# Optimization experiments

Hardware: AMD Instinct MI355X
Metric: run time of the kernel (lower is better)

## Reference

```python
import jax, jax.numpy as jnp
import numpy as np
import math

NUM_CLASSES = 100000
EMBED = 384
BATCH = 512
S = 64.0
M = 0.5
COS_M = math.cos(M)
SIN_M = math.sin(M)
TH = math.cos(math.pi - M)
MM = math.sin(math.pi - M) * M
EPS = 1e-07


def setup_inputs() -> dict:
    key = jax.random.key(0)
    k1, k2, k3 = jax.random.split(key, 3)
    embeddings = jax.random.normal(k1, (BATCH, EMBED), dtype=jnp.float32)
    labels = jax.random.randint(k2, (BATCH,), 0, NUM_CLASSES, dtype=jnp.int64)
    # xavier_uniform-like init for weight [num_classes, embedding_size]
    limit = math.sqrt(6.0 / (NUM_CLASSES + EMBED))
    weight = jax.random.uniform(k3, (NUM_CLASSES, EMBED), dtype=jnp.float32,
                                minval=-limit, maxval=limit)
    return {"embeddings": embeddings, "labels": labels, "weight": weight}


def reference(embeddings, labels, weight):
    # normalize class weights (note: embeddings are NOT normalized, per source)
    W = weight / jnp.linalg.norm(weight, axis=1, keepdims=True)  # [C, E]
    cos_theta = jnp.clip(embeddings @ W.T, -1.0 + EPS, 1.0 - EPS)  # [B, C]
    sin_theta = jnp.sqrt(1.0 - cos_theta ** 2)
    cos_theta_m = cos_theta * COS_M - sin_theta * SIN_M
    cos_theta_m = jnp.where(cos_theta > TH, cos_theta_m, cos_theta - MM)
    one_hot = jax.nn.one_hot(labels, cos_theta.shape[1], dtype=cos_theta.dtype)
    logits = S * (one_hot * cos_theta_m + (1.0 - one_hot) * cos_theta)
    # mean cross-entropy
    logp = jax.nn.log_softmax(logits, axis=-1)  # [B, C]
    nll = -jnp.take_along_axis(logp, labels[:, None], axis=1)[:, 0]
    return jnp.mean(nll)
```

## Files before the change

kernel.cpp:

```cpp
#include <hip/hip_runtime.h>
#include <hip/hip_bf16.h>
#include <math.h>

#define C_CLASSES 100000
#define EMBED     384
#define BATCH     512
#define S_SCALE   64.0f
#define COS_M_    0.8775825618903728f
#define SIN_M_    0.479425538604203f
#define TH_       (-0.8775825618903728f)
#define MM_       0.2397127693021015f
#define EPS_      1e-7f
#define LOG2E_    1.4426950408889634f
#define LN2_      0.6931471805599453f
#define BIGZ_     92.33261191693459f
#define SK1_      92.33248f

#define CT    32
#define NCHK  3125
#define NBLK  (NCHK * 2)

typedef __attribute__((ext_vector_type(8))) short bf16x8;
typedef __attribute__((ext_vector_type(4))) float f32x4;

__device__ inline ushort f2bf(float f) {
    unsigned u = __float_as_uint(f);
    unsigned r = (u + 0x7fffu + ((u >> 16) & 1u)) >> 16;
    return (ushort)r;
}

__global__ __launch_bounds__(256)
void cvt_pack_e(const float* __restrict__ emb, ushort* __restrict__ eP)
{
    int t = blockIdx.x * 256 + threadIdx.x;
    int lane = t & 63;
    int grp  = t >> 6;
    int tile = grp / 12, ks = grp % 12;
    int lr = lane & 15, lg = lane >> 4;
    int row = tile * 16 + lr;
    int col = ks * 32 + lg * 8;
    const float4* src = (const float4*)(emb + (size_t)row * EMBED + col);
    float4 v0 = src[0], v1 = src[1];
    ushort4 o0, o1;
    o0.x = f2bf(v0.x); o0.y = f2bf(v0.y); o0.z = f2bf(v0.z); o0.w = f2bf(v0.w);
    o1.x = f2bf(v1.x); o1.y = f2bf(v1.y); o1.z = f2bf(v1.z); o1.w = f2bf(v1.w);
    ((ushort4*)eP)[t * 2]     = o0;
    ((ushort4*)eP)[t * 2 + 1] = o1;
}

__global__ __launch_bounds__(256, 5)
void arc_fused32(const ushort* __restrict__ eP, const int* __restrict__ labels,
                 const float* __restrict__ weight,
                 float* __restrict__ psum, float* __restrict__ zlabel)
{
    __shared__ ushort Bl[(CT / 16) * 12 * 512];
    __shared__ int    labL[256];

    const int tid = threadIdx.x;

    const int orig = blockIdx.x;
    const int xcd  = orig & 7;
    const int qq   = NBLK >> 3, rr = NBLK & 7;
    const int bid  = (xcd < rr ? xcd * (qq + 1)
                               : rr * (qq + 1) + (xcd - rr) * qq) + (orig >> 3);
    const int ck   = bid >> 1;
    const int mh   = bid & 1;
    const int c0   = ck * CT;

    labL[tid] = labels[mh * 256 + tid];

    {
        const int p = tid & 15;
        #pragma unroll
        for (int h = 0; h < 2; ++h) {
            const int c = h * 16 + (tid >> 4);
            const float4* src =
                (const float4*)(weight + (size_t)(c0 + c) * EMBED) + p;

            float4 wv[6];
            float ss = 0.f;
            #pragma unroll
            for (int i = 0; i < 6; ++i) {
                wv[i] = src[16 * i];
                ss += wv[i].x * wv[i].x + wv[i].y * wv[i].y
                    + wv[i].z * wv[i].z + wv[i].w * wv[i].w;
            }
            ss += __shfl_xor(ss, 1, 64);
            ss += __shfl_xor(ss, 2, 64);
            ss += __shfl_xor(ss, 4, 64);
            ss += __shfl_xor(ss, 8, 64);
            const float inv = (ss > 0.f) ? rsqrtf(ss) : 0.f;

            const int t2 = c >> 4, cl = c & 15;
            #pragma unroll
            for (int i = 0; i < 6; ++i) {
                int q   = p + 16 * i;
                int ks  = q >> 3;
                int lgp = (q >> 1) & 3;
                int jo  = (q & 1) * 4;
                ushort4 o;
                o.x = f2bf(wv[i].x * inv); o.y = f2bf(wv[i].y * inv);
                o.z = f2bf(wv[i].z * inv); o.w = f2bf(wv[i].w * inv);
                int ei = (((t2 * 12 + ks) * 64) + cl + 16 * lgp) * 8 + jo;
                ei ^= (lgp & 3) << 4;
                *(ushort4*)&Bl[ei] = o;
            }
            __builtin_amdgcn_sched_barrier(0);
        }
    }
    __syncthreads();

    const int wid = tid >> 6, l = tid & 63;
    const int lr  = l & 15,  lg = l >> 4;
    const int bxo = (lg & 3) << 4;

    const ushort* abase = eP + ((size_t)((mh * 16 + wid * 4) * 12) * 64 + l) * 8;

    f32x4 acc[4][2];
    #pragma unroll
    for (int mt = 0; mt < 4; ++mt) {
        acc[mt][0] = (f32x4){0.f, 0.f, 0.f, 0.f};
        acc[mt][1] = (f32x4){0.f, 0.f, 0.f, 0.f};
    }

    #pragma unroll
    for (int ks = 0; ks < 12; ++ks) {
        bf16x8 a[4], b[2];
        #pragma unroll
        for (int mt = 0; mt < 4; ++mt)
            a[mt] = *(const bf16x8*)(abase + (mt * 12 + ks) * 512);
        #pragma unroll
        for (int nt = 0; nt < 2; ++nt) {
            int ei = ((nt * 12 + ks) * 64 + l) * 8;
            b[nt] = *(const bf16x8*)&Bl[ei ^ bxo];
        }
        #pragma unroll
        for (int mt = 0; mt < 4; ++mt) {
            acc[mt][0] = __builtin_amdgcn_mfma_f32_16x16x32_bf16(
                a[mt], b[0], acc[mt][0], 0, 0, 0);
            acc[mt][1] = __builtin_amdgcn_mfma_f32_16x16x32_bf16(
                a[mt], b[1], acc[mt][1], 0, 0, 0);
        }
    }

    #pragma unroll
    for (int mt = 0; mt < 4; ++mt) {
        #pragma unroll
        for (int rg = 0; rg < 4; ++rg) {
            const int rl  = wid * 64 + mt * 16 + lg * 4 + rg;
            const int r   = mh * 256 + rl;
            const int lab = labL[rl];
            float acc4 = 0.f;
            #pragma unroll
            for (int nt = 0; nt < 2; ++nt) {
                float cv = acc[mt][nt][rg];
                cv = fminf(fmaxf(cv, -1.f + EPS_), 1.f - EPS_);
                acc4 += exp2f(fmaf(cv, SK1_, -BIGZ_));
            }
            int off = lab - c0;
            if (((unsigned)off < 32u) && ((off & 15) == lr)) {
                float cv = (off >> 4) ? acc[mt][1][rg] : acc[mt][0][rg];
                cv = fminf(fmaxf(cv, -1.f + EPS_), 1.f - EPS_);
                float plain = exp2f(fmaf(cv, SK1_, -BIGZ_));
                float zm;
                if (cv > TH_) {
                    float sv = sqrtf(fmaxf(1.f - cv * cv, 0.f));
                    zm = S_SCALE * (cv * COS_M_ - sv * SIN_M_);
                } else {
                    zm = S_SCALE * (cv - MM_);
                }
                acc4 += exp2f(fmaf(zm, LOG2E_, -BIGZ_)) - plain;
                zlabel[r] = zm;
            }
            acc4 += __shfl_xor(acc4, 1, 64);
            acc4 += __shfl_xor(acc4, 2, 64);
            acc4 += __shfl_xor(acc4, 4, 64);
            acc4 += __shfl_xor(acc4, 8, 64);
            if (lr == 0) psum[(size_t)ck * BATCH + r] = acc4;
        }
    }
}

__global__ __launch_bounds__(256)
void arc_reduce(const float* __restrict__ psum, const float* __restrict__ zlabel,
                float* __restrict__ rowloss)
{
    const int r = blockIdx.x;
    const int tid = threadIdx.x;
    float s = 0.f;
    for (int k = tid; k < NCHK; k += 256)
        s += psum[(size_t)k * BATCH + r];
    #pragma unroll
    for (int d = 1; d < 64; d <<= 1) s += __shfl_xor(s, d, 64);
    __shared__ float ssh[4];
    if ((tid & 63) == 0) ssh[tid >> 6] = s;
    __syncthreads();
    if (tid == 0) {
        float t = ssh[0] + ssh[1] + ssh[2] + ssh[3];
        rowloss[r] = LN2_ * (BIGZ_ + log2f(t)) - zlabel[r];
    }
}

__global__ __launch_bounds__(512)
void arc_mean(const float* __restrict__ rowloss, float* __restrict__ out)
{
    const int tid = threadIdx.x;
    float v = rowloss[tid];
    #pragma unroll
    for (int d = 1; d < 64; d <<= 1) v += __shfl_xor(v, d, 64);
    __shared__ float sv[8];
    if ((tid & 63) == 0) sv[tid >> 6] = v;
    __syncthreads();
    if (tid == 0) {
        float t = 0.f;
        #pragma unroll
        for (int w = 0; w < 8; ++w) t += sv[w];
        out[0] = t / (float)BATCH;
    }
}

extern "C" void kernel_launch(void* const* d_in, const int* in_sizes, int n_in,
                              void* d_out, int out_size, void* d_ws, size_t ws_size,
                              hipStream_t stream)
{
    (void)in_sizes; (void)n_in; (void)out_size; (void)ws_size;
    const float* emb    = (const float*)d_in[0];
    const int*   labels = (const int*)d_in[1];
    const float* weight = (const float*)d_in[2];
    float* out = (float*)d_out;

    float*  psum    = (float*)d_ws;
    float*  zlabel  = psum + (size_t)NCHK * BATCH;
    float*  rowloss = zlabel + BATCH;
    ushort* eP      = (ushort*)(rowloss + BATCH);

    cvt_pack_e<<<(BATCH * EMBED / 8) / 256, 256, 0, stream>>>(emb, eP);
    arc_fused32<<<NBLK, 256, 0, stream>>>(eP, labels, weight, psum, zlabel);
    arc_reduce<<<BATCH, 256, 0, stream>>>(psum, zlabel, rowloss);
    arc_mean<<<1, 512, 0, stream>>>(rowloss, out);
}
```

Before: 102.6 us.

## Make weight GEMM kernel persistent with double-buffered global-to-LDS prefetch

Replaces the 6250-block one-shot kernel with 256 persistent blocks of 512 threads. Each block loops over class chunks and covers all 512 batch rows per chunk. Weight chunks are streamed straight into LDS with global_load_lds into two buffers, so the next chunk loads while the current one is normalised and multiplied. This is meant to hide global memory latency and cut launch and redundant weight-normalisation overhead. In exchange it uses about 124KB of LDS per block, which leaves one block per CU and relies on hand-placed waitcnt and barrier ordering. It also swaps the manual bf16 rounding for the library conversion.

```diff
diff --git a/kernel.cpp b/kernel.cpp
--- a/kernel.cpp
+++ b/kernel.cpp
@@ -18,15 +18,23 @@
 
 #define CT    32
 #define NCHK  3125
-#define NBLK  (NCHK * 2)
+#define NB    256
 
 typedef __attribute__((ext_vector_type(8))) short bf16x8;
 typedef __attribute__((ext_vector_type(4))) float f32x4;
+
+#define AS1 __attribute__((address_space(1)))
+#define AS3 __attribute__((address_space(3)))
 
 __device__ inline ushort f2bf(float f) {
     unsigned u = __float_as_uint(f);
     unsigned r = (u + 0x7fffu + ((u >> 16) & 1u)) >> 16;
     return (ushort)r;
+}
+
+__device__ inline ushort cvt_bf(float f) {
+    __hip_bfloat16 h = __float2bfloat16(f);
+    return *(ushort*)&h;
 }
 
 __global__ __launch_bounds__(256)
@@ -48,40 +56,60 @@
     ((ushort4*)eP)[t * 2 + 1] = o1;
 }
 
-__global__ __launch_bounds__(256, 5)
-void arc_fused32(const ushort* __restrict__ eP, const int* __restrict__ labels,
-                 const float* __restrict__ weight,
-                 float* __restrict__ psum, float* __restrict__ zlabel)
-{
+__global__ __launch_bounds__(512, 4)
+void arc_pipe32(const ushort* __restrict__ eP, const int* __restrict__ labels,
+                const float* __restrict__ weight,
+                float* __restrict__ psum, float* __restrict__ zlabel)
+{
+    __shared__ float  Raw[2][CT * EMBED];
     __shared__ ushort Bl[(CT / 16) * 12 * 512];
-    __shared__ int    labL[256];
+    __shared__ int    labL[BATCH];
 
     const int tid = threadIdx.x;
-
-    const int orig = blockIdx.x;
-    const int xcd  = orig & 7;
-    const int qq   = NBLK >> 3, rr = NBLK & 7;
-    const int bid  = (xcd < rr ? xcd * (qq + 1)
-                               : rr * (qq + 1) + (xcd - rr) * qq) + (orig >> 3);
-    const int ck   = bid >> 1;
-    const int mh   = bid & 1;
-    const int c0   = ck * CT;
-
-    labL[tid] = labels[mh * 256 + tid];
-
-    {
-        const int p = tid & 15;
-        #pragma unroll
-        for (int h = 0; h < 2; ++h) {
-            const int c = h * 16 + (tid >> 4);
-            const float4* src =
-                (const float4*)(weight + (size_t)(c0 + c) * EMBED) + p;
-
+    const int blk = blockIdx.x;
+    const int nch = 12 + ((blk < (NCHK - 12 * NB)) ? 1 : 0);
+
+    labL[tid] = labels[tid];
+
+    const int c  = tid >> 4, p = tid & 15;
+    const int t2 = c >> 4,  cl = c & 15;
+    const int wid = tid >> 6, l = tid & 63;
+    const int lr  = l & 15,  lg = l >> 4;
+    const int bxo = (lg & 3) << 4;
+    const ushort* abase = eP + ((size_t)(wid * 4) * 12 * 64 + l) * 8;
+
+#define DMA(CH, BUF) do {                                                     \
+        const AS1 uint* g_ = (const AS1 uint*)weight                          \
+                           + (size_t)(CH) * (CT * EMBED);                     \
+        _Pragma("unroll")                                                     \
+        for (int j_ = 0; j_ < 6; ++j_) {                                      \
+            const AS1 uint* gp_ = g_ + (size_t)(j_ * 512 + tid) * 4;          \
+            AS3 uint* lp_ = (AS3 uint*)&Raw[BUF][0]                           \
+                          + (size_t)(j_ * 512 + (tid & ~63)) * 4;             \
+            __builtin_amdgcn_global_load_lds(gp_, lp_, 16, 0, 0);             \
+        }                                                                     \
+    } while (0)
+
+    DMA(blk, 0);
+    DMA(blk + NB, 1);
+
+    int ck = blk;
+    for (int k = 0; k < nch; ++k) {
+        const int cur = k & 1;
+        const int c0  = ck * CT;
+
+        asm volatile("s_waitcnt vmcnt(6)" ::: "memory");
+        __builtin_amdgcn_sched_barrier(0);
+        __builtin_amdgcn_s_barrier();
+        __builtin_amdgcn_sched_barrier(0);
+
+        {
+            const float4* rp = (const float4*)&Raw[cur][(size_t)c * EMBED];
             float4 wv[6];
             float ss = 0.f;
             #pragma unroll
             for (int i = 0; i < 6; ++i) {
-                wv[i] = src[16 * i];
+                wv[i] = rp[p + 16 * i];
                 ss += wv[i].x * wv[i].x + wv[i].y * wv[i].y
                     + wv[i].z * wv[i].z + wv[i].w * wv[i].w;
             }
@@ -91,7 +119,6 @@
             ss += __shfl_xor(ss, 8, 64);
             const float inv = (ss > 0.f) ? rsqrtf(ss) : 0.f;
 
-            const int t2 = c >> 4, cl = c & 15;
             #pragma unroll
             for (int i = 0; i < 6; ++i) {
                 int q   = p + 16 * i;
@@ -99,86 +126,87 @@
                 int lgp = (q >> 1) & 3;
                 int jo  = (q & 1) * 4;
                 ushort4 o;
-                o.x = f2bf(wv[i].x * inv); o.y = f2bf(wv[i].y * inv);
-                o.z = f2bf(wv[i].z * inv); o.w = f2bf(wv[i].w * inv);
+                o.x = cvt_bf(wv[i].x * inv); o.y = cvt_bf(wv[i].y * inv);
+                o.z = cvt_bf(wv[i].z * inv); o.w = cvt_bf(wv[i].w * inv);
                 int ei = (((t2 * 12 + ks) * 64) + cl + 16 * lgp) * 8 + jo;
                 ei ^= (lgp & 3) << 4;
                 *(ushort4*)&Bl[ei] = o;
             }
-            __builtin_amdgcn_sched_barrier(0);
-        }
+        }
+        asm volatile("s_waitcnt lgkmcnt(0)" ::: "memory");
+        __builtin_amdgcn_sched_barrier(0);
+        __builtin_amdgcn_s_barrier();
+        __builtin_amdgcn_sched_barrier(0);
+
+        f32x4 acc[4][2];
+        #pragma unroll
+        for (int mt = 0; mt < 4; ++mt) {
+            acc[mt][0] = (f32x4){0.f, 0.f, 0.f, 0.f};
+            acc[mt][1] = (f32x4){0.f, 0.f, 0.f, 0.f};
+        }
+
+        #pragma unroll
+        for (int ks = 0; ks < 12; ++ks) {
+            bf16x8 a[4], b[2];
+            #pragma unroll
+            for (int mt = 0; mt < 4; ++mt)
+                a[mt] = *(const bf16x8*)(abase + (mt * 12 + ks) * 512);
+            #pragma unroll
+            for (int nt = 0; nt < 2; ++nt) {
+                int ei = ((nt * 12 + ks) * 64 + l) * 8;
+                b[nt] = *(const bf16x8*)&Bl[ei ^ bxo];
+            }
+            #pragma unroll
+            for (int mt = 0; mt < 4; ++mt) {
+                acc[mt][0] = __builtin_amdgcn_mfma_f32_16x16x32_bf16(
+                    a[mt], b[0], acc[mt][0], 0, 0, 0);
+                acc[mt][1] = __builtin_amdgcn_mfma_f32_16x16x32_bf16(
+                    a[mt], b[1], acc[mt][1], 0, 0, 0);
+            }
+        }
+
+        #pragma unroll
+        for (int mt = 0; mt < 4; ++mt) {
+            #pragma unroll
+            for (int rg = 0; rg < 4; ++rg) {
+                const int r   = wid * 64 + mt * 16 + lg * 4 + rg;
+                const int lab = labL[r];
+                float acc4 = 0.f;
+                #pragma unroll
+                for (int nt = 0; nt < 2; ++nt) {
+                    float cv = acc[mt][nt][rg];
+                    cv = fminf(fmaxf(cv, -1.f + EPS_), 1.f - EPS_);
+                    acc4 += exp2f(fmaf(cv, SK1_, -BIGZ_));
+                }
+                int off = lab - c0;
+                if (((unsigned)off < 32u) && ((off & 15) == lr)) {
+                    float cv = (off >> 4) ? acc[mt][1][rg] : acc[mt][0][rg];
+                    cv = fminf(fmaxf(cv, -1.f + EPS_), 1.f - EPS_);
+                    float plain = exp2f(fmaf(cv, SK1_, -BIGZ_));
+                    float zm;
+                    if (cv > TH_) {
+                        float sv = sqrtf(fmaxf(1.f - cv * cv, 0.f));
+                        zm = S_SCALE * (cv * COS_M_ - sv * SIN_M_);
+                    } else {
+                        zm = S_SCALE * (cv - MM_);
+                    }
+                    acc4 += exp2f(fmaf(zm, LOG2E_, -BIGZ_)) - plain;
+                    zlabel[r] = zm;
+                }
+                acc4 += __shfl_xor(acc4, 1, 64);
+                acc4 += __shfl_xor(acc4, 2, 64);
+                acc4 += __shfl_xor(acc4, 4, 64);
+                acc4 += __shfl_xor(acc4, 8, 64);
+                if (lr == 0) psum[(size_t)ck * BATCH + r] = acc4;
+            }
+        }
+
+        if (k + 2 < nch) DMA(ck + 2 * NB, cur);
+        __builtin_amdgcn_sched_barrier(0);
+
+        ck += NB;
     }
-    __syncthreads();
-
-    const int wid = tid >> 6, l = tid & 63;
-    const int lr  = l & 15,  lg = l >> 4;
-    const int bxo = (lg & 3) << 4;
-
-    const ushort* abase = eP + ((size_t)((mh * 16 + wid * 4) * 12) * 64 + l) * 8;
-
-    f32x4 acc[4][2];
-    #pragma unroll
-    for (int mt = 0; mt < 4; ++mt) {
-        acc[mt][0] = (f32x4){0.f, 0.f, 0.f, 0.f};
-        acc[mt][1] = (f32x4){0.f, 0.f, 0.f, 0.f};
-    }
-
-    #pragma unroll
-    for (int ks = 0; ks < 12; ++ks) {
-        bf16x8 a[4], b[2];
-        #pragma unroll
-        for (int mt = 0; mt < 4; ++mt)
-            a[mt] = *(const bf16x8*)(abase + (mt * 12 + ks) * 512);
-        #pragma unroll
-        for (int nt = 0; nt < 2; ++nt) {
-            int ei = ((nt * 12 + ks) * 64 + l) * 8;
-            b[nt] = *(const bf16x8*)&Bl[ei ^ bxo];
-        }
-        #pragma unroll
-        for (int mt = 0; mt < 4; ++mt) {
-            acc[mt][0] = __builtin_amdgcn_mfma_f32_16x16x32_bf16(
-                a[mt], b[0], acc[mt][0], 0, 0, 0);
-            acc[mt][1] = __builtin_amdgcn_mfma_f32_16x16x32_bf16(
-                a[mt], b[1], acc[mt][1], 0, 0, 0);
-        }
-    }
-
-    #pragma unroll
-    for (int mt = 0; mt < 4; ++mt) {
-        #pragma unroll
-        for (int rg = 0; rg < 4; ++rg) {
-            const int rl  = wid * 64 + mt * 16 + lg * 4 + rg;
-            const int r   = mh * 256 + rl;
-            const int lab = labL[rl];
-            float acc4 = 0.f;
-            #pragma unroll
-            for (int nt = 0; nt < 2; ++nt) {
-                float cv = acc[mt][nt][rg];
-                cv = fminf(fmaxf(cv, -1.f + EPS_), 1.f - EPS_);
-                acc4 += exp2f(fmaf(cv, SK1_, -BIGZ_));
-            }
-            int off = lab - c0;
-            if (((unsigned)off < 32u) && ((off & 15) == lr)) {
-                float cv = (off >> 4) ? acc[mt][1][rg] : acc[mt][0][rg];
-                cv = fminf(fmaxf(cv, -1.f + EPS_), 1.f - EPS_);
-                float plain = exp2f(fmaf(cv, SK1_, -BIGZ_));
-                float zm;
-                if (cv > TH_) {
-                    float sv = sqrtf(fmaxf(1.f - cv * cv, 0.f));
-                    zm = S_SCALE * (cv * COS_M_ - sv * SIN_M_);
-                } else {
-                    zm = S_SCALE * (cv - MM_);
-                }
-                acc4 += exp2f(fmaf(zm, LOG2E_, -BIGZ_)) - plain;
-                zlabel[r] = zm;
-            }
-            acc4 += __shfl_xor(acc4, 1, 64);
-            acc4 += __shfl_xor(acc4, 2, 64);
-            acc4 += __shfl_xor(acc4, 4, 64);
-            acc4 += __shfl_xor(acc4, 8, 64);
-            if (lr == 0) psum[(size_t)ck * BATCH + r] = acc4;
-        }
-    }
+#undef DMA
 }
 
 __global__ __launch_bounds__(256)
@@ -235,7 +263,7 @@
     ushort* eP      = (ushort*)(rowloss + BATCH);
 
     cvt_pack_e<<<(BATCH * EMBED / 8) / 256, 256, 0, stream>>>(emb, eP);
-    arc_fused32<<<NBLK, 256, 0, stream>>>(eP, labels, weight, psum, zlabel);
+    arc_pipe32<<<NB, 512, 0, stream>>>(eP, labels, weight, psum, zlabel);
     arc_reduce<<<BATCH, 256, 0, stream>>>(psum, zlabel, rowloss);
     arc_mean<<<1, 512, 0, stream>>>(rowloss, out);
 }
```

Result: slower. 135.4 us (+32.0%).
